# Kernel optimization log

Measured on AMD Instinct MI355X. Metric: run time of the kernel, lower is better.

## Reference

```python
import jax, jax.numpy as jnp
import numpy as np

NF = 64      # feature channels
DG = 8       # deformable groups
K = 9        # 3x3 kernel taps


def conv3(x, w, b):
    # 3x3 conv, stride 1, pad 1, NCHW/OIHW
    y = jax.lax.conv_general_dilated(x, w, (1, 1), ((1, 1), (1, 1)),
                                     dimension_numbers=('NCHW', 'OIHW', 'NCHW'))
    return y + b[None, :, None, None]


def lrelu(x):
    return jnp.where(x >= 0, x, 0.1 * x)


def up2(x):
    # matches F.interpolate(scale_factor=2, mode='bilinear', align_corners=False)
    b, c, h, w = x.shape
    return jax.image.resize(x, (b, c, 2 * h, 2 * w), method='bilinear')


def _sample_group(img, py, px):
    # img: [Cg,H,W]; py,px: [K,H,W] absolute float sample coords; zero pad outside
    H, W = img.shape[-2:]
    y0 = jnp.floor(py)
    x0 = jnp.floor(px)
    wy = py - y0
    wx = px - x0
    y0i = y0.astype(jnp.int32)
    x0i = x0.astype(jnp.int32)

    def gather(yi, xi):
        valid = (yi >= 0) & (yi < H) & (xi >= 0) & (xi < W)
        yc = jnp.clip(yi, 0, H - 1)
        xc = jnp.clip(xi, 0, W - 1)
        return img[:, yc, xc] * valid[None].astype(img.dtype)  # [Cg,K,H,W]

    v00 = gather(y0i, x0i)
    v01 = gather(y0i, x0i + 1)
    v10 = gather(y0i + 1, x0i)
    v11 = gather(y0i + 1, x0i + 1)
    return (1 - wy) * ((1 - wx) * v00 + wx * v01) + wy * ((1 - wx) * v10 + wx * v11)


def dcn_sep(x, off_fea, om_w, om_b, w, b):
    # DCN_sep: conv_offset_mask(off_fea) -> (o1,o2,mask); modulated deformable 3x3 conv on x
    B, C, H, W = x.shape
    om = conv3(off_fea, om_w, om_b)                       # [B, 3*DG*K, H, W]
    o1, o2, m = jnp.split(om, 3, axis=1)
    off_y = o1.reshape(B, DG, K, H, W)
    off_x = o2.reshape(B, DG, K, H, W)
    mask = jax.nn.sigmoid(m).reshape(B, DG, K, H, W)

    k = jnp.arange(3, dtype=x.dtype) - 1.0
    dy = jnp.repeat(k, 3)   # [K] row-major kernel offsets
    dx = jnp.tile(k, 3)
    hh = jnp.arange(H, dtype=x.dtype)
    ww = jnp.arange(W, dtype=x.dtype)
    py = off_y + dy[:, None, None] + hh[None, :, None]    # [B,DG,K,H,W]
    px = off_x + dx[:, None, None] + ww[None, None, :]

    xg = x.reshape(B, DG, C // DG, H, W)
    samp = jax.vmap(jax.vmap(_sample_group))(xg, py, px)  # [B,DG,Cg,K,H,W]
    samp = (samp * mask[:, :, None]).reshape(B, C, K, H, W)
    wk = w.reshape(w.shape[0], C, K)                      # [O,C,9]
    return jnp.einsum('ock,bckhw->bohw', wk, samp) + b[None, :, None, None]


def setup_inputs() -> dict:
    key = jax.random.key(0)
    ks = jax.random.split(key, 16)
    d = {
        'fea1_l1': jax.random.normal(ks[0], (4, NF, 128, 128), jnp.float32),
        'fea1_l2': jax.random.normal(ks[1], (4, NF, 64, 64), jnp.float32),
        'fea1_l3': jax.random.normal(ks[2], (4, NF, 32, 32), jnp.float32),
        'fea2_l1': jax.random.normal(ks[3], (4, NF, 128, 128), jnp.float32),
        'fea2_l2': jax.random.normal(ks[4], (4, NF, 64, 64), jnp.float32),
        'fea2_l3': jax.random.normal(ks[5], (4, NF, 32, 32), jnp.float32),
        # 8 plain 3x3 convs with in=2*nf: [L3_off1, L2_off1, L2_off2, L2_fea, L1_off1, L1_off2, L1_fea, cas_off1]
        'w128': jax.random.normal(ks[6], (8, NF, 2 * NF, 3, 3), jnp.float32) * 0.05,
        'b128': jax.random.normal(ks[7], (8, NF), jnp.float32) * 0.01,
        # 4 plain 3x3 convs with in=nf: [L3_off2, L2_off3, L1_off3, cas_off2]
        'w64': jax.random.normal(ks[8], (4, NF, NF, 3, 3), jnp.float32) * 0.05,
        'b64': jax.random.normal(ks[9], (4, NF), jnp.float32) * 0.01,
        # 4 DCN_sep modules: [L3, L2, L1, cas]
        'om_w': jax.random.normal(ks[10], (4, 3 * DG * K, NF, 3, 3), jnp.float32) * 0.01,
        'om_b': jax.random.normal(ks[11], (4, 3 * DG * K), jnp.float32) * 0.01,
        'dcn_w': jax.random.normal(ks[12], (4, NF, NF, 3, 3), jnp.float32) * 0.05,
        'dcn_b': jax.random.normal(ks[13], (4, NF), jnp.float32) * 0.01,
    }
    return d


def reference(fea1_l1, fea1_l2, fea1_l3, fea2_l1, fea2_l2, fea2_l3,
              w128, b128, w64, b64, om_w, om_b, dcn_w, dcn_b):
    cat = lambda a, b_: jnp.concatenate([a, b_], axis=1)
    # L3
    L3_off = lrelu(conv3(cat(fea1_l3, fea2_l3), w128[0], b128[0]))
    L3_off = lrelu(conv3(L3_off, w64[0], b64[0]))
    L3_fea = lrelu(dcn_sep(fea1_l3, L3_off, om_w[0], om_b[0], dcn_w[0], dcn_b[0]))
    # L2
    L2_off = lrelu(conv3(cat(fea1_l2, fea2_l2), w128[1], b128[1]))
    L3_off_up = up2(L3_off)
    L2_off = lrelu(conv3(cat(L2_off, L3_off_up * 2), w128[2], b128[2]))
    L2_off = lrelu(conv3(L2_off, w64[1], b64[1]))
    L2_fea = dcn_sep(fea1_l2, L2_off, om_w[1], om_b[1], dcn_w[1], dcn_b[1])
    L3_fea_up = up2(L3_fea)
    L2_fea = lrelu(conv3(cat(L2_fea, L3_fea_up), w128[3], b128[3]))
    # L1
    L1_off = lrelu(conv3(cat(fea1_l1, fea2_l1), w128[4], b128[4]))
    L2_off_up = up2(L2_off)
    L1_off = lrelu(conv3(cat(L1_off, L2_off_up * 2), w128[5], b128[5]))
    L1_off = lrelu(conv3(L1_off, w64[2], b64[2]))
    L1_fea = dcn_sep(fea1_l1, L1_off, om_w[2], om_b[2], dcn_w[2], dcn_b[2])
    L2_fea_up = up2(L2_fea)
    L1_fea = conv3(cat(L1_fea, L2_fea_up), w128[6], b128[6])
    # Cascading
    off = lrelu(conv3(cat(L1_fea, fea2_l1), w128[7], b128[7]))
    off = lrelu(conv3(off, w64[3], b64[3]))
    return lrelu(dcn_sep(L1_fea, off, om_w[3], om_b[3], dcn_w[3], dcn_b[3]))
```

## Files before the change

kernel.cpp:

```cpp
#include <hip/hip_runtime.h>
#include <cstdint>
#include <cstddef>


typedef __bf16 bf16x8 __attribute__((ext_vector_type(8)));
typedef float  f32x4  __attribute__((ext_vector_type(4)));

template<int OCPAD, int C>
__global__ void wsplit_k(const float* __restrict__ src, __bf16* __restrict__ dst,
                         int OC, long total)
{
    const int per = 9 * OCPAD * C;
    long i = (long)blockIdx.x * 256 + threadIdx.x;
    if (i >= total) return;
    int n  = (int)(i / per);
    int r  = (int)(i - (long)n * per);
    int t  = r / (OCPAD * C);
    int r2 = r - t * (OCPAD * C);
    int o  = r2 / C;
    int c  = r2 - o * C;
    float v = (o < OC) ? src[(((long)n * OC + o) * C + c) * 9 + t] : 0.f;
    __bf16 h = (__bf16)v;
    __bf16 l = (__bf16)(v - (float)h);
    __bf16* d = dst + (long)n * 2 * per;
    d[r]       = h;
    d[per + r] = l;
}

__global__ void transpose_dcnw(const float* __restrict__ w, float* __restrict__ wt, long total)
{
    long i = (long)blockIdx.x * 256 + threadIdx.x;
    if (i >= total) return;
    int n = (int)(i / 36864);
    int r = (int)(i % 36864);
    int o = r / 576;
    int c = (r % 576) / 9;
    int k = r % 9;
    wt[(long)n * 36864 + ((size_t)k * 64 + c) * 64 + o] = w[i];
}

template<int C1, int C2, int NMT, int OCPAD, bool RELU>
__global__ __launch_bounds__(256)
void conv_mfma_k(const float* __restrict__ in1, const float* __restrict__ in2,
                 float scale2, const __bf16* __restrict__ wt, const float* __restrict__ bg,
                 float* __restrict__ out, int H, int W, int OCtot)
{
    constexpr int C = C1 + C2;
    constexpr int PER = 9 * OCPAD * C;
    constexpr int NCHUNK = OCPAD / (NMT * 16);
    const int bz = blockIdx.z;
    const int b = bz / NCHUNK, chunk = bz - b * NCHUNK;
    const int ocblk = chunk * NMT * 16;
    const int tid = threadIdx.x;
    const int wid = __builtin_amdgcn_readfirstlane(tid >> 6);
    const int lane = tid & 63;
    const int pix = lane & 15;
    const int oct = lane >> 4;
    const int h0 = blockIdx.y * 8, w0 = blockIdx.x * 8;
    const size_t HW = (size_t)H * W;

    __shared__ __bf16 XH[100 * 40];
    __shared__ __bf16 XL[100 * 40];

    f32x4 accm[NMT], accc[NMT];
#pragma unroll
    for (int mt = 0; mt < NMT; ++mt) { accm[mt] = f32x4{0,0,0,0}; accc[mt] = f32x4{0,0,0,0}; }

    const int py = 2 * wid + (pix >> 3), px = pix & 7;
    const int pixbase = (py * 10 + px) * 40 + oct * 8;
    const int alane = (lane & 15) * C + oct * 8;

    for (int c0 = 0; c0 < C; c0 += 32) {
        __syncthreads();
        for (int task = tid; task < 400; task += 256) {
            int p  = task >> 2, o8 = (task & 3) * 8;
            int y  = p / 10, x = p - y * 10;
            int gy = h0 + y - 1, gx = w0 + x - 1;
            bool valid = (gy >= 0) & (gy < H) & (gx >= 0) & (gx < W);
            int cc = c0 + o8;
            const float* src; float sc;
            if (C2 == 0 || cc < C1) { src = in1 + ((size_t)b * C1 + cc) * HW; sc = 1.f; }
            else                    { src = in2 + ((size_t)b * C2 + (cc - C1)) * HW; sc = scale2; }
            const size_t gofs = (size_t)gy * W + gx;
            bf16x8 hv, lv;
#pragma unroll
            for (int j = 0; j < 8; ++j) {
                float v = valid ? src[(size_t)j * HW + gofs] * sc : 0.f;
                __bf16 h = (__bf16)v;
                hv[j] = h;
                lv[j] = (__bf16)(v - (float)h);
            }
            *(bf16x8*)(&XH[p * 40 + o8]) = hv;
            *(bf16x8*)(&XL[p * 40 + o8]) = lv;
        }
        __syncthreads();

#pragma unroll
        for (int dy = 0; dy < 3; ++dy) {
#pragma unroll
            for (int dx = 0; dx < 3; ++dx) {
                const int t = dy * 3 + dx;
                const int loff = pixbase + (dy * 10 + dx) * 40;
                bf16x8 bh = *(const bf16x8*)(&XH[loff]);
                bf16x8 bl = *(const bf16x8*)(&XL[loff]);
                const __bf16* wbase = wt + (size_t)(t * OCPAD + ocblk) * C + c0 + alane;
#pragma unroll
                for (int mt = 0; mt < NMT; ++mt) {
                    bf16x8 ah = *(const bf16x8*)(wbase + mt * 16 * C);
                    bf16x8 al = *(const bf16x8*)(wbase + mt * 16 * C + PER);
                    accm[mt] = __builtin_amdgcn_mfma_f32_16x16x32_bf16(ah, bh, accm[mt], 0, 0, 0);
                    accc[mt] = __builtin_amdgcn_mfma_f32_16x16x32_bf16(ah, bl, accc[mt], 0, 0, 0);
                    accc[mt] = __builtin_amdgcn_mfma_f32_16x16x32_bf16(al, bh, accc[mt], 0, 0, 0);
                }
            }
        }
    }

    const int orow4 = oct * 4;
    float* obase = out + (size_t)b * OCtot * HW + (size_t)(h0 + py) * W + (w0 + px);
#pragma unroll
    for (int mt = 0; mt < NMT; ++mt) {
#pragma unroll
        for (int j = 0; j < 4; ++j) {
            int oc = ocblk + mt * 16 + orow4 + j;
            if (oc < OCtot) {
                float r = accm[mt][j] + accc[mt][j] + bg[oc];
                if (RELU) r = (r >= 0.f) ? r : 0.1f * r;
                obase[(size_t)oc * HW] = r;
            }
        }
    }
}

template<bool RELU>
__global__ __launch_bounds__(256)
void dcn_k(const float* __restrict__ x, const float* __restrict__ om,
           const float* __restrict__ Wt, const float* __restrict__ bg,
           float* __restrict__ out, int H, int W)
{
    const int b = blockIdx.z;
    const int tid = threadIdx.x;
    const int wid = __builtin_amdgcn_readfirstlane(tid >> 6);
    const int p = tid & 63;
    const int h = blockIdx.y * 8 + (p >> 3), w = blockIdx.x * 8 + (p & 7);
    const size_t HW = (size_t)H * W;

    float acc[64];
#pragma unroll
    for (int o = 0; o < 64; ++o) acc[o] = 0.f;

    const float* omb = om + (size_t)b * 216 * HW + (size_t)h * W + w;
    const float* xb  = x + (size_t)b * 64 * HW;

    for (int gg = 0; gg < 2; ++gg) {
        const int g = wid * 2 + gg;
        for (int k = 0; k < 9; ++k) {
            const int ch = g * 9 + k;
            float oy = omb[(size_t)ch * HW];
            float ox = omb[(size_t)(72 + ch) * HW];
            float mr = omb[(size_t)(144 + ch) * HW];
            float m  = 1.f / (1.f + expf(-mr));

            float pyf = oy + (float)(k / 3 - 1) + (float)h;
            float pxf = ox + (float)(k % 3 - 1) + (float)w;
            float fy = floorf(pyf), fx = floorf(pxf);
            float wy = pyf - fy, wx = pxf - fx;
            int y0 = (int)fy, x0 = (int)fx;
            int y1 = y0 + 1, x1 = x0 + 1;
            bool vy0 = (y0 >= 0) & (y0 < H), vy1 = (y1 >= 0) & (y1 < H);
            bool vx0 = (x0 >= 0) & (x0 < W), vx1 = (x1 >= 0) & (x1 < W);
            int y0c = y0 < 0 ? 0 : (y0 >= H ? H - 1 : y0);
            int y1c = y1 < 0 ? 0 : (y1 >= H ? H - 1 : y1);
            int x0c = x0 < 0 ? 0 : (x0 >= W ? W - 1 : x0);
            int x1c = x1 < 0 ? 0 : (x1 >= W ? W - 1 : x1);
            float w00 = (1.f - wy) * (1.f - wx) * m * ((vy0 & vx0) ? 1.f : 0.f);
            float w01 = (1.f - wy) * wx         * m * ((vy0 & vx1) ? 1.f : 0.f);
            float w10 = wy         * (1.f - wx) * m * ((vy1 & vx0) ? 1.f : 0.f);
            float w11 = wy         * wx         * m * ((vy1 & vx1) ? 1.f : 0.f);
            size_t i00 = (size_t)y0c * W + x0c, i01 = (size_t)y0c * W + x1c;
            size_t i10 = (size_t)y1c * W + x0c, i11 = (size_t)y1c * W + x1c;

            float s[8];
#pragma unroll
            for (int cg = 0; cg < 8; ++cg) {
                const float* xc = xb + (size_t)(g * 8 + cg) * HW;
                s[cg] = w00 * xc[i00] + w01 * xc[i01] + w10 * xc[i10] + w11 * xc[i11];
            }
#pragma unroll
            for (int cg = 0; cg < 8; ++cg) {
                const float* wko = Wt + ((size_t)k * 64 + g * 8 + cg) * 64;
                float sv = s[cg];
#pragma unroll
                for (int o = 0; o < 64; ++o)
                    acc[o] = fmaf(wko[o], sv, acc[o]);
            }
        }
    }

    __shared__ float red[3][64][65];
    if (wid > 0) {
#pragma unroll
        for (int o = 0; o < 64; ++o) red[wid - 1][p][o] = acc[o];
    }
    __syncthreads();
    if (wid == 0) {
#pragma unroll
        for (int o = 0; o < 64; ++o)
            acc[o] += red[0][p][o] + red[1][p][o] + red[2][p][o];
        float* op = out + ((size_t)b * 64) * HW + (size_t)h * W + w;
#pragma unroll
        for (int o = 0; o < 64; ++o) {
            float r = acc[o] + bg[o];
            if (RELU) r = (r >= 0.f) ? r : 0.1f * r;
            op[(size_t)o * HW] = r;
        }
    }
}

__global__ void up2_k(const float* __restrict__ in, float* __restrict__ out,
                      int H, int W, long total)
{
    long idx = (long)blockIdx.x * 256 + threadIdx.x;
    if (idx >= total) return;
    const int W2 = 2 * W, H2 = 2 * H;
    int w2 = (int)(idx % W2);
    long t = idx / W2;
    int h2 = (int)(t % H2);
    long bc = t / H2;
    const float* src = in + bc * (size_t)H * W;
    int jx = w2 >> 1, jy = h2 >> 1;
    int x0, y0; float wx0, wy0;
    if (w2 & 1) { x0 = jx;     wx0 = 0.75f; } else { x0 = jx - 1; wx0 = 0.25f; }
    if (h2 & 1) { y0 = jy;     wy0 = 0.75f; } else { y0 = jy - 1; wy0 = 0.25f; }
    int x1 = x0 + 1 > W - 1 ? W - 1 : x0 + 1;
    int y1 = y0 + 1 > H - 1 ? H - 1 : y0 + 1;
    if (x0 < 0) x0 = 0;
    if (y0 < 0) y0 = 0;
    float v00 = src[(size_t)y0 * W + x0], v01 = src[(size_t)y0 * W + x1];
    float v10 = src[(size_t)y1 * W + x0], v11 = src[(size_t)y1 * W + x1];
    float wx1 = 1.f - wx0, wy1 = 1.f - wy0;
    out[idx] = wy0 * (wx0 * v00 + wx1 * v01) + wy1 * (wx0 * v10 + wx1 * v11);
}

extern "C" void kernel_launch(void* const* d_in, const int* in_sizes, int n_in,
                              void* d_out, int out_size, void* d_ws, size_t ws_size,
                              hipStream_t stream)
{
    const float* fea1_l1 = (const float*)d_in[0];
    const float* fea1_l2 = (const float*)d_in[1];
    const float* fea1_l3 = (const float*)d_in[2];
    const float* fea2_l1 = (const float*)d_in[3];
    const float* fea2_l2 = (const float*)d_in[4];
    const float* fea2_l3 = (const float*)d_in[5];
    const float* w128  = (const float*)d_in[6];
    const float* b128  = (const float*)d_in[7];
    const float* w64   = (const float*)d_in[8];
    const float* b64   = (const float*)d_in[9];
    const float* om_w  = (const float*)d_in[10];
    const float* om_b  = (const float*)d_in[11];
    const float* dcn_w = (const float*)d_in[12];
    const float* dcn_b = (const float*)d_in[13];
    float* outp = (float*)d_out;

    float* ws = (float*)d_ws;
    const size_t S1  = (size_t)4 * 64 * 128 * 128;
    const size_t S2  = (size_t)4 * 64 * 64 * 64;
    const size_t S3  = (size_t)4 * 64 * 32 * 32;
    const size_t ASZ = (size_t)4 * 216 * 128 * 128;
    float* A  = ws;
    float* Bb = ws + S1;
    float* Cb = ws + 2 * S1;
    float* Db = ws + 3 * S1;
    float* sA = ws + 4 * S1;
    float* sG = sA + ASZ - 2 * S2;
    float* sH = sA + ASZ - S2;
    float* dT = sA + ASZ;

    __bf16* U = (__bf16*)d_out;
    __bf16* w128T = U;
    __bf16* w64T  = U + 1179648;
    __bf16* omT   = U + 1474560;

    float* e3a = A;   float* e3b = A + S3;   float* e3c = A + 2 * S3;
    float* f2a = Bb;  float* f2b = Bb + S2;  float* f2c = Bb + 2 * S2;

    const dim3 blk(256);

    {
        long t1 = 8l * 73728;
        wsplit_k<64,128><<<(int)((t1 + 255) / 256), 256, 0, stream>>>(w128, w128T, 64, t1);
        long t2 = 4l * 36864;
        wsplit_k<64,64><<<(int)((t2 + 255) / 256), 256, 0, stream>>>(w64, w64T, 64, t2);
        long t3 = 4l * 129024;
        wsplit_k<224,64><<<(int)((t3 + 255) / 256), 256, 0, stream>>>(om_w, omT, 216, t3);
        transpose_dcnw<<<(int)((4l * 36864 + 255) / 256), 256, 0, stream>>>(dcn_w, dT, 4l * 36864);
    }

    conv_mfma_k<64,64,4,64,true ><<<dim3(4,4,4), blk, 0, stream>>>(fea1_l3, fea2_l3, 1.f, w128T + 0l*147456, b128 + 0*64, e3a, 32, 32, 64);
    conv_mfma_k<64, 0,4,64,true ><<<dim3(4,4,4), blk, 0, stream>>>(e3a, nullptr, 1.f, w64T + 0l*73728, b64 + 0*64, e3b, 32, 32, 64);
    conv_mfma_k<64, 0,7,224,false><<<dim3(4,4,8), blk, 0, stream>>>(e3b, nullptr, 1.f, omT + 0l*258048, om_b + 0*216, sA, 32, 32, 216);
    dcn_k<true ><<<dim3(4,4,4), blk, 0, stream>>>(fea1_l3, sA, dT + 0*36864, dcn_b + 0*64, e3c, 32, 32);

    conv_mfma_k<64,64,4,64,true ><<<dim3(8,8,4), blk, 0, stream>>>(fea1_l2, fea2_l2, 1.f, w128T + 1l*147456, b128 + 1*64, f2a, 64, 64, 64);
    up2_k<<<(int)((S2 + 255) / 256), 256, 0, stream>>>(e3b, f2b, 32, 32, (long)S2);
    conv_mfma_k<64,64,4,64,true ><<<dim3(8,8,4), blk, 0, stream>>>(f2a, f2b, 2.f, w128T + 2l*147456, b128 + 2*64, f2c, 64, 64, 64);
    conv_mfma_k<64, 0,4,64,true ><<<dim3(8,8,4), blk, 0, stream>>>(f2c, nullptr, 1.f, w64T + 1l*73728, b64 + 1*64, sG, 64, 64, 64);
    conv_mfma_k<64, 0,7,224,false><<<dim3(8,8,8), blk, 0, stream>>>(sG, nullptr, 1.f, omT + 1l*258048, om_b + 1*216, sA, 64, 64, 216);
    dcn_k<false><<<dim3(8,8,4), blk, 0, stream>>>(fea1_l2, sA, dT + 1*36864, dcn_b + 1*64, f2a, 64, 64);
    up2_k<<<(int)((S2 + 255) / 256), 256, 0, stream>>>(e3c, f2b, 32, 32, (long)S2);
    conv_mfma_k<64,64,4,64,true ><<<dim3(8,8,4), blk, 0, stream>>>(f2a, f2b, 1.f, w128T + 3l*147456, b128 + 3*64, sH, 64, 64, 64);

    conv_mfma_k<64,64,4,64,true ><<<dim3(16,16,4), blk, 0, stream>>>(fea1_l1, fea2_l1, 1.f, w128T + 4l*147456, b128 + 4*64, A, 128, 128, 64);
    up2_k<<<(int)((S1 + 255) / 256), 256, 0, stream>>>(sG, Bb, 64, 64, (long)S1);
    conv_mfma_k<64,64,4,64,true ><<<dim3(16,16,4), blk, 0, stream>>>(A, Bb, 2.f, w128T + 5l*147456, b128 + 5*64, Cb, 128, 128, 64);
    conv_mfma_k<64, 0,4,64,true ><<<dim3(16,16,4), blk, 0, stream>>>(Cb, nullptr, 1.f, w64T + 2l*73728, b64 + 2*64, A, 128, 128, 64);
    up2_k<<<(int)((S1 + 255) / 256), 256, 0, stream>>>(sH, Bb, 64, 64, (long)S1);
    conv_mfma_k<64, 0,7,224,false><<<dim3(16,16,8), blk, 0, stream>>>(A, nullptr, 1.f, omT + 2l*258048, om_b + 2*216, sA, 128, 128, 216);
    dcn_k<false><<<dim3(16,16,4), blk, 0, stream>>>(fea1_l1, sA, dT + 2*36864, dcn_b + 2*64, Cb, 128, 128);
    conv_mfma_k<64,64,4,64,false><<<dim3(16,16,4), blk, 0, stream>>>(Cb, Bb, 1.f, w128T + 6l*147456, b128 + 6*64, Db, 128, 128, 64);

    conv_mfma_k<64,64,4,64,true ><<<dim3(16,16,4), blk, 0, stream>>>(Db, fea2_l1, 1.f, w128T + 7l*147456, b128 + 7*64, A, 128, 128, 64);
    conv_mfma_k<64, 0,4,64,true ><<<dim3(16,16,4), blk, 0, stream>>>(A, nullptr, 1.f, w64T + 3l*73728, b64 + 3*64, Bb, 128, 128, 64);
    conv_mfma_k<64, 0,7,224,false><<<dim3(16,16,8), blk, 0, stream>>>(Bb, nullptr, 1.f, omT + 3l*258048, om_b + 3*216, sA, 128, 128, 216);
    dcn_k<true ><<<dim3(16,16,4), blk, 0, stream>>>(Db, sA, dT + 3*36864, dcn_b + 3*64, outp, 128, 128);
}
```

Measured before the change: 2.438 ms.

## Switch intermediates to NHWC split-bf16 and drop LDS staging in conv

All intermediate activations are converted once to NHWC hi/lo bf16 pairs. The conv kernel now loads MFMA operands straight from global memory with contiguous 8-channel vectors instead of staging and splitting fp32 NCHW tiles in LDS. Upsample, DCN sampling and the offset conv output also use NHWC, so the DCN gathers 8 channels per corner in one vector load. The aim is to remove the repeated fp32-to-bf16 split and the strided NCHW gathers, at the cost of extra conversion kernels, a reworked workspace layout, and losing the 3x3 halo reuse that LDS used to provide.

```diff
diff --git a/kernel.cpp b/kernel.cpp
--- a/kernel.cpp
+++ b/kernel.cpp
@@ -4,6 +4,7 @@
 
 
 typedef __bf16 bf16x8 __attribute__((ext_vector_type(8)));
+typedef __bf16 bf16x4 __attribute__((ext_vector_type(4)));
 typedef float  f32x4  __attribute__((ext_vector_type(4)));
 
 template<int OCPAD, int C>
@@ -39,126 +40,200 @@
     wt[(long)n * 36864 + ((size_t)k * 64 + c) * 64 + o] = w[i];
 }
 
-template<int C1, int C2, int NMT, int OCPAD, bool RELU>
+__global__ void tobf_k(const float* __restrict__ in, __bf16* __restrict__ out,
+                       long npl, int HW, long total)
+{
+    long idx = (long)blockIdx.x * 256 + threadIdx.x;
+    if (idx >= total) return;
+    int  p  = (int)(idx % HW);
+    long r  = idx / HW;
+    int  o8 = ((int)(r & 7)) * 8;
+    int  b  = (int)(r >> 3);
+    const float* src = in + ((long)b * 64 + o8) * HW + p;
+    long obase = ((long)b * HW + p) * 64 + o8;
+    bf16x8 hv, lv;
+#pragma unroll
+    for (int j = 0; j < 8; ++j) {
+        float v = src[(long)j * HW];
+        __bf16 h = (__bf16)v;
+        hv[j] = h;
+        lv[j] = (__bf16)(v - (float)h);
+    }
+    *(bf16x8*)(out + obase) = hv;
+    *(bf16x8*)(out + npl + obase) = lv;
+}
+
+__global__ void up2_nhwc_k(const __bf16* __restrict__ in, long inpl,
+                           __bf16* __restrict__ out, long outpl,
+                           int H, int W, float scale, long total)
+{
+    long idx = (long)blockIdx.x * 256 + threadIdx.x;
+    if (idx >= total) return;
+    int o8 = ((int)(idx & 7)) * 8;
+    long t = idx >> 3;
+    const int W2 = 2 * W, H2 = 2 * H;
+    int ox = (int)(t % W2); t /= W2;
+    int oy = (int)(t % H2);
+    int b  = (int)(t / H2);
+    int jx = ox >> 1, jy = oy >> 1;
+    int x0, y0; float wx0, wy0;
+    if (ox & 1) { x0 = jx;     wx0 = 0.75f; } else { x0 = jx - 1; wx0 = 0.25f; }
+    if (oy & 1) { y0 = jy;     wy0 = 0.75f; } else { y0 = jy - 1; wy0 = 0.25f; }
+    int x1 = x0 + 1 > W - 1 ? W - 1 : x0 + 1;
+    int y1 = y0 + 1 > H - 1 ? H - 1 : y0 + 1;
+    if (x0 < 0) x0 = 0;
+    if (y0 < 0) y0 = 0;
+    float v00[8], v01[8], v10[8], v11[8];
+    auto ld = [&](int yy, int xx, float* v) {
+        long bo = ((long)(b * H + yy) * W + xx) * 64 + o8;
+        bf16x8 hh = *(const bf16x8*)(in + bo);
+        bf16x8 ll = *(const bf16x8*)(in + inpl + bo);
+#pragma unroll
+        for (int j = 0; j < 8; ++j) v[j] = (float)hh[j] + (float)ll[j];
+    };
+    ld(y0, x0, v00); ld(y0, x1, v01); ld(y1, x0, v10); ld(y1, x1, v11);
+    float wx1 = 1.f - wx0, wy1 = 1.f - wy0;
+    long obo = ((long)(b * H2 + oy) * W2 + ox) * 64 + o8;
+    bf16x8 ho, lo_;
+#pragma unroll
+    for (int j = 0; j < 8; ++j) {
+        float r = (wy0 * (wx0 * v00[j] + wx1 * v01[j]) +
+                   wy1 * (wx0 * v10[j] + wx1 * v11[j])) * scale;
+        __bf16 h = (__bf16)r;
+        ho[j]  = h;
+        lo_[j] = (__bf16)(r - (float)h);
+    }
+    *(bf16x8*)(out + obo) = ho;
+    *(bf16x8*)(out + outpl + obo) = lo_;
+}
+
+template<int C, int NMT, int OCPAD, int OCTOT, bool RELU, bool OUTF32>
 __global__ __launch_bounds__(256)
-void conv_mfma_k(const float* __restrict__ in1, const float* __restrict__ in2,
-                 float scale2, const __bf16* __restrict__ wt, const float* __restrict__ bg,
-                 float* __restrict__ out, int H, int W, int OCtot)
-{
-    constexpr int C = C1 + C2;
+void conv_nhwc_k(const __bf16* __restrict__ in1, const __bf16* __restrict__ in2,
+                 long nplane, const __bf16* __restrict__ wt, const float* __restrict__ bg,
+                 void* __restrict__ outv, long onplane, int H, int W)
+{
     constexpr int PER = 9 * OCPAD * C;
-    constexpr int NCHUNK = OCPAD / (NMT * 16);
-    const int bz = blockIdx.z;
-    const int b = bz / NCHUNK, chunk = bz - b * NCHUNK;
+    const int chunk = blockIdx.z;
     const int ocblk = chunk * NMT * 16;
     const int tid = threadIdx.x;
     const int wid = __builtin_amdgcn_readfirstlane(tid >> 6);
     const int lane = tid & 63;
-    const int pix = lane & 15;
-    const int oct = lane >> 4;
-    const int h0 = blockIdx.y * 8, w0 = blockIdx.x * 8;
-    const size_t HW = (size_t)H * W;
-
-    __shared__ __bf16 XH[100 * 40];
-    __shared__ __bf16 XL[100 * 40];
-
-    f32x4 accm[NMT], accc[NMT];
-#pragma unroll
-    for (int mt = 0; mt < NMT; ++mt) { accm[mt] = f32x4{0,0,0,0}; accc[mt] = f32x4{0,0,0,0}; }
-
-    const int py = 2 * wid + (pix >> 3), px = pix & 7;
-    const int pixbase = (py * 10 + px) * 40 + oct * 8;
-    const int alane = (lane & 15) * C + oct * 8;
+    const int pix = lane & 15, oct = lane >> 4;
+    const int by = blockIdx.y * 4 + wid;
+    const int b = by / H, y = by - b * H;
+    const int x0 = blockIdx.x * 16;
+    const int x = x0 + pix;
+
+    int xoff[3]; bool vxm[3];
+#pragma unroll
+    for (int dx = 0; dx < 3; ++dx) {
+        int gx = x + dx - 1;
+        bool v = (gx >= 0) & (gx < W);
+        vxm[dx] = v;
+        int gc = v ? gx : (gx < 0 ? 0 : W - 1);
+        xoff[dx] = gc * 64;
+    }
+
+    f32x4 am[NMT], ac[NMT];
+#pragma unroll
+    for (int mt = 0; mt < NMT; ++mt) { am[mt] = f32x4{0,0,0,0}; ac[mt] = f32x4{0,0,0,0}; }
+
+    const bf16x8 zv = bf16x8{};
+    const int coctB = oct * 8;
 
     for (int c0 = 0; c0 < C; c0 += 32) {
-        __syncthreads();
-        for (int task = tid; task < 400; task += 256) {
-            int p  = task >> 2, o8 = (task & 3) * 8;
-            int y  = p / 10, x = p - y * 10;
-            int gy = h0 + y - 1, gx = w0 + x - 1;
-            bool valid = (gy >= 0) & (gy < H) & (gx >= 0) & (gx < W);
-            int cc = c0 + o8;
-            const float* src; float sc;
-            if (C2 == 0 || cc < C1) { src = in1 + ((size_t)b * C1 + cc) * HW; sc = 1.f; }
-            else                    { src = in2 + ((size_t)b * C2 + (cc - C1)) * HW; sc = scale2; }
-            const size_t gofs = (size_t)gy * W + gx;
-            bf16x8 hv, lv;
-#pragma unroll
-            for (int j = 0; j < 8; ++j) {
-                float v = valid ? src[(size_t)j * HW + gofs] * sc : 0.f;
-                __bf16 h = (__bf16)v;
-                hv[j] = h;
-                lv[j] = (__bf16)(v - (float)h);
-            }
-            *(bf16x8*)(&XH[p * 40 + o8]) = hv;
-            *(bf16x8*)(&XL[p * 40 + o8]) = lv;
+        const __bf16* src = (C == 64 || c0 < 64) ? in1 : in2;
+        const int csub = (C == 64) ? c0 : (c0 & 63);
+        const __bf16* srcl = src + nplane;
+        const int cofs = csub + coctB;
+#pragma unroll
+        for (int r = 0; r < 3; ++r) {
+            int gy = y + r - 1;
+            if (gy < 0 || gy >= H) continue;
+            long rb = ((long)(b * H + gy) * W) * 64 + cofs;
+            bf16x8 bh[3], bl[3];
+#pragma unroll
+            for (int dx = 0; dx < 3; ++dx) {
+                bf16x8 h = *(const bf16x8*)(src  + rb + xoff[dx]);
+                bf16x8 l = *(const bf16x8*)(srcl + rb + xoff[dx]);
+                bh[dx] = vxm[dx] ? h : zv;
+                bl[dx] = vxm[dx] ? l : zv;
+            }
+#pragma unroll
+            for (int dx = 0; dx < 3; ++dx) {
+                const int t = r * 3 + dx;
+                const __bf16* wb = wt + ((long)t * OCPAD + ocblk + pix) * C + c0 + coctB;
+#pragma unroll
+                for (int mt = 0; mt < NMT; ++mt) {
+                    bf16x8 ah = *(const bf16x8*)(wb + (long)mt * 16 * C);
+                    bf16x8 al = *(const bf16x8*)(wb + (long)mt * 16 * C + PER);
+                    am[mt] = __builtin_amdgcn_mfma_f32_16x16x32_bf16(ah, bh[dx], am[mt], 0, 0, 0);
+                    ac[mt] = __builtin_amdgcn_mfma_f32_16x16x32_bf16(ah, bl[dx], ac[mt], 0, 0, 0);
+                    ac[mt] = __builtin_amdgcn_mfma_f32_16x16x32_bf16(al, bh[dx], ac[mt], 0, 0, 0);
+                }
+            }
         }
-        __syncthreads();
-
-#pragma unroll
-        for (int dy = 0; dy < 3; ++dy) {
-#pragma unroll
-            for (int dx = 0; dx < 3; ++dx) {
-                const int t = dy * 3 + dx;
-                const int loff = pixbase + (dy * 10 + dx) * 40;
-                bf16x8 bh = *(const bf16x8*)(&XH[loff]);
-                bf16x8 bl = *(const bf16x8*)(&XL[loff]);
-                const __bf16* wbase = wt + (size_t)(t * OCPAD + ocblk) * C + c0 + alane;
-#pragma unroll
-                for (int mt = 0; mt < NMT; ++mt) {
-                    bf16x8 ah = *(const bf16x8*)(wbase + mt * 16 * C);
-                    bf16x8 al = *(const bf16x8*)(wbase + mt * 16 * C + PER);
-                    accm[mt] = __builtin_amdgcn_mfma_f32_16x16x32_bf16(ah, bh, accm[mt], 0, 0, 0);
-                    accc[mt] = __builtin_amdgcn_mfma_f32_16x16x32_bf16(ah, bl, accc[mt], 0, 0, 0);
-                    accc[mt] = __builtin_amdgcn_mfma_f32_16x16x32_bf16(al, bh, accc[mt], 0, 0, 0);
-                }
+    }
+
+    if (OUTF32) {
+        float* outf = (float*)outv;
+        long opix = ((long)(b * H + y) * W + x) * (long)OCTOT;
+#pragma unroll
+        for (int mt = 0; mt < NMT; ++mt) {
+#pragma unroll
+            for (int j = 0; j < 4; ++j) {
+                int oc = ocblk + mt * 16 + oct * 4 + j;
+                if (oc < OCTOT) outf[opix + oc] = am[mt][j] + ac[mt][j] + bg[oc];
             }
         }
-    }
-
-    const int orow4 = oct * 4;
-    float* obase = out + (size_t)b * OCtot * HW + (size_t)(h0 + py) * W + (w0 + px);
-#pragma unroll
-    for (int mt = 0; mt < NMT; ++mt) {
-#pragma unroll
-        for (int j = 0; j < 4; ++j) {
-            int oc = ocblk + mt * 16 + orow4 + j;
-            if (oc < OCtot) {
-                float r = accm[mt][j] + accc[mt][j] + bg[oc];
-                if (RELU) r = (r >= 0.f) ? r : 0.1f * r;
-                obase[(size_t)oc * HW] = r;
-            }
+    } else {
+        __bf16* outp = (__bf16*)outv;
+        long opix = ((long)(b * H + y) * W + x) * 64;
+#pragma unroll
+        for (int mt = 0; mt < NMT; ++mt) {
+            int oc0 = ocblk + mt * 16 + oct * 4;
+            bf16x4 hv, lv;
+#pragma unroll
+            for (int j = 0; j < 4; ++j) {
+                float rv = am[mt][j] + ac[mt][j] + bg[oc0 + j];
+                if (RELU) rv = (rv >= 0.f) ? rv : 0.1f * rv;
+                __bf16 hh = (__bf16)rv;
+                hv[j] = hh;
+                lv[j] = (__bf16)(rv - (float)hh);
+            }
+            *(bf16x4*)(outp + opix + oc0) = hv;
+            *(bf16x4*)(outp + onplane + opix + oc0) = lv;
         }
     }
 }
 
-template<bool RELU>
+template<bool RELU, bool OUTF32>
 __global__ __launch_bounds__(256)
-void dcn_k(const float* __restrict__ x, const float* __restrict__ om,
-           const float* __restrict__ Wt, const float* __restrict__ bg,
-           float* __restrict__ out, int H, int W)
+void dcn_nhwc_k(const __bf16* __restrict__ x, long xnpl,
+                const float* __restrict__ om,
+                const float* __restrict__ Wt, const float* __restrict__ bg,
+                void* __restrict__ outv, long onpl, int H, int W)
 {
     const int b = blockIdx.z;
     const int tid = threadIdx.x;
     const int wid = __builtin_amdgcn_readfirstlane(tid >> 6);
     const int p = tid & 63;
     const int h = blockIdx.y * 8 + (p >> 3), w = blockIdx.x * 8 + (p & 7);
-    const size_t HW = (size_t)H * W;
 
     float acc[64];
 #pragma unroll
     for (int o = 0; o < 64; ++o) acc[o] = 0.f;
 
-    const float* omb = om + (size_t)b * 216 * HW + (size_t)h * W + w;
-    const float* xb  = x + (size_t)b * 64 * HW;
+    const float* omp = om + ((long)(b * H + h) * W + w) * 216;
 
     for (int gg = 0; gg < 2; ++gg) {
         const int g = wid * 2 + gg;
         for (int k = 0; k < 9; ++k) {
             const int ch = g * 9 + k;
-            float oy = omb[(size_t)ch * HW];
-            float ox = omb[(size_t)(72 + ch) * HW];
-            float mr = omb[(size_t)(144 + ch) * HW];
+            float oy = omp[ch];
+            float ox = omp[72 + ch];
+            float mr = omp[144 + ch];
             float m  = 1.f / (1.f + expf(-mr));
 
             float pyf = oy + (float)(k / 3 - 1) + (float)h;
@@ -177,18 +252,28 @@
             float w01 = (1.f - wy) * wx         * m * ((vy0 & vx1) ? 1.f : 0.f);
             float w10 = wy         * (1.f - wx) * m * ((vy1 & vx0) ? 1.f : 0.f);
             float w11 = wy         * wx         * m * ((vy1 & vx1) ? 1.f : 0.f);
-            size_t i00 = (size_t)y0c * W + x0c, i01 = (size_t)y0c * W + x1c;
-            size_t i10 = (size_t)y1c * W + x0c, i11 = (size_t)y1c * W + x1c;
+
+            long i00 = ((long)(b * H + y0c) * W + x0c) * 64 + g * 8;
+            long i01 = ((long)(b * H + y0c) * W + x1c) * 64 + g * 8;
+            long i10 = ((long)(b * H + y1c) * W + x0c) * 64 + g * 8;
+            long i11 = ((long)(b * H + y1c) * W + x1c) * 64 + g * 8;
+
+            bf16x8 h00 = *(const bf16x8*)(x + i00), l00 = *(const bf16x8*)(x + xnpl + i00);
+            bf16x8 h01 = *(const bf16x8*)(x + i01), l01 = *(const bf16x8*)(x + xnpl + i01);
+            bf16x8 h10 = *(const bf16x8*)(x + i10), l10 = *(const bf16x8*)(x + xnpl + i10);
+            bf16x8 h11 = *(const bf16x8*)(x + i11), l11 = *(const bf16x8*)(x + xnpl + i11);
 
             float s[8];
 #pragma unroll
+            for (int j = 0; j < 8; ++j) {
+                s[j] = w00 * ((float)h00[j] + (float)l00[j])
+                     + w01 * ((float)h01[j] + (float)l01[j])
+                     + w10 * ((float)h10[j] + (float)l10[j])
+                     + w11 * ((float)h11[j] + (float)l11[j]);
+            }
+#pragma unroll
             for (int cg = 0; cg < 8; ++cg) {
-                const float* xc = xb + (size_t)(g * 8 + cg) * HW;
-                s[cg] = w00 * xc[i00] + w01 * xc[i01] + w10 * xc[i10] + w11 * xc[i11];
-            }
-#pragma unroll
-            for (int cg = 0; cg < 8; ++cg) {
-                const float* wko = Wt + ((size_t)k * 64 + g * 8 + cg) * 64;
+                const float* wko = Wt + ((long)k * 64 + g * 8 + cg) * 64;
                 float sv = s[cg];
 #pragma unroll
                 for (int o = 0; o < 64; ++o)
@@ -207,39 +292,34 @@
 #pragma unroll
         for (int o = 0; o < 64; ++o)
             acc[o] += red[0][p][o] + red[1][p][o] + red[2][p][o];
-        float* op = out + ((size_t)b * 64) * HW + (size_t)h * W + w;
-#pragma unroll
-        for (int o = 0; o < 64; ++o) {
-            float r = acc[o] + bg[o];
-            if (RELU) r = (r >= 0.f) ? r : 0.1f * r;
-            op[(size_t)o * HW] = r;
+        if (OUTF32) {
+            const long HW = (long)H * W;
+            float* op = (float*)outv + ((long)b * 64) * HW + (long)h * W + w;
+#pragma unroll
+            for (int o = 0; o < 64; ++o) {
+                float r = acc[o] + bg[o];
+                if (RELU) r = (r >= 0.f) ? r : 0.1f * r;
+                op[(long)o * HW] = r;
+            }
+        } else {
+            __bf16* op = (__bf16*)outv;
+            long obo = ((long)(b * H + h) * W + w) * 64;
+#pragma unroll
+            for (int o0 = 0; o0 < 64; o0 += 8) {
+                bf16x8 hv, lv;
+#pragma unroll
+                for (int j = 0; j < 8; ++j) {
+                    float r = acc[o0 + j] + bg[o0 + j];
+                    if (RELU) r = (r >= 0.f) ? r : 0.1f * r;
+                    __bf16 hh = (__bf16)r;
+                    hv[j] = hh;
+                    lv[j] = (__bf16)(r - (float)hh);
+                }
+                *(bf16x8*)(op + obo + o0) = hv;
+                *(bf16x8*)(op + onpl + obo + o0) = lv;
+            }
         }
     }
-}
-
-__global__ void up2_k(const float* __restrict__ in, float* __restrict__ out,
-                      int H, int W, long total)
-{
-    long idx = (long)blockIdx.x * 256 + threadIdx.x;
-    if (idx >= total) return;
-    const int W2 = 2 * W, H2 = 2 * H;
-    int w2 = (int)(idx % W2);
-    long t = idx / W2;
-    int h2 = (int)(t % H2);
-    long bc = t / H2;
-    const float* src = in + bc * (size_t)H * W;
-    int jx = w2 >> 1, jy = h2 >> 1;
-    int x0, y0; float wx0, wy0;
-    if (w2 & 1) { x0 = jx;     wx0 = 0.75f; } else { x0 = jx - 1; wx0 = 0.25f; }
-    if (h2 & 1) { y0 = jy;     wy0 = 0.75f; } else { y0 = jy - 1; wy0 = 0.25f; }
-    int x1 = x0 + 1 > W - 1 ? W - 1 : x0 + 1;
-    int y1 = y0 + 1 > H - 1 ? H - 1 : y0 + 1;
-    if (x0 < 0) x0 = 0;
-    if (y0 < 0) y0 = 0;
-    float v00 = src[(size_t)y0 * W + x0], v01 = src[(size_t)y0 * W + x1];
-    float v10 = src[(size_t)y1 * W + x0], v11 = src[(size_t)y1 * W + x1];
-    float wx1 = 1.f - wx0, wy1 = 1.f - wy0;
-    out[idx] = wy0 * (wx0 * v00 + wx1 * v01) + wy1 * (wx0 * v10 + wx1 * v11);
 }
 
 extern "C" void kernel_launch(void* const* d_in, const int* in_sizes, int n_in,
@@ -260,67 +340,94 @@
     const float* om_b  = (const float*)d_in[11];
     const float* dcn_w = (const float*)d_in[12];
     const float* dcn_b = (const float*)d_in[13];
-    float* outp = (float*)d_out;
-
+
+    const long NPL1 = 4194304, NPL2 = 1048576, NPL3 = 262144;
     float* ws = (float*)d_ws;
-    const size_t S1  = (size_t)4 * 64 * 128 * 128;
-    const size_t S2  = (size_t)4 * 64 * 64 * 64;
-    const size_t S3  = (size_t)4 * 64 * 32 * 32;
-    const size_t ASZ = (size_t)4 * 216 * 128 * 128;
-    float* A  = ws;
-    float* Bb = ws + S1;
-    float* Cb = ws + 2 * S1;
-    float* Db = ws + 3 * S1;
-    float* sA = ws + 4 * S1;
-    float* sG = sA + ASZ - 2 * S2;
-    float* sH = sA + ASZ - S2;
-    float* dT = sA + ASZ;
-
-    __bf16* U = (__bf16*)d_out;
-    __bf16* w128T = U;
-    __bf16* w64T  = U + 1179648;
-    __bf16* omT   = U + 1474560;
-
-    float* e3a = A;   float* e3b = A + S3;   float* e3c = A + 2 * S3;
-    float* f2a = Bb;  float* f2b = Bb + S2;  float* f2c = Bb + 2 * S2;
-
-    const dim3 blk(256);
-
-    {
-        long t1 = 8l * 73728;
-        wsplit_k<64,128><<<(int)((t1 + 255) / 256), 256, 0, stream>>>(w128, w128T, 64, t1);
-        long t2 = 4l * 36864;
-        wsplit_k<64,64><<<(int)((t2 + 255) / 256), 256, 0, stream>>>(w64, w64T, 64, t2);
-        long t3 = 4l * 129024;
-        wsplit_k<224,64><<<(int)((t3 + 255) / 256), 256, 0, stream>>>(om_w, omT, 216, t3);
-        transpose_dcnw<<<(int)((4l * 36864 + 255) / 256), 256, 0, stream>>>(dcn_w, dT, 4l * 36864);
-    }
-
-    conv_mfma_k<64,64,4,64,true ><<<dim3(4,4,4), blk, 0, stream>>>(fea1_l3, fea2_l3, 1.f, w128T + 0l*147456, b128 + 0*64, e3a, 32, 32, 64);
-    conv_mfma_k<64, 0,4,64,true ><<<dim3(4,4,4), blk, 0, stream>>>(e3a, nullptr, 1.f, w64T + 0l*73728, b64 + 0*64, e3b, 32, 32, 64);
-    conv_mfma_k<64, 0,7,224,false><<<dim3(4,4,8), blk, 0, stream>>>(e3b, nullptr, 1.f, omT + 0l*258048, om_b + 0*216, sA, 32, 32, 216);
-    dcn_k<true ><<<dim3(4,4,4), blk, 0, stream>>>(fea1_l3, sA, dT + 0*36864, dcn_b + 0*64, e3c, 32, 32);
-
-    conv_mfma_k<64,64,4,64,true ><<<dim3(8,8,4), blk, 0, stream>>>(fea1_l2, fea2_l2, 1.f, w128T + 1l*147456, b128 + 1*64, f2a, 64, 64, 64);
-    up2_k<<<(int)((S2 + 255) / 256), 256, 0, stream>>>(e3b, f2b, 32, 32, (long)S2);
-    conv_mfma_k<64,64,4,64,true ><<<dim3(8,8,4), blk, 0, stream>>>(f2a, f2b, 2.f, w128T + 2l*147456, b128 + 2*64, f2c, 64, 64, 64);
-    conv_mfma_k<64, 0,4,64,true ><<<dim3(8,8,4), blk, 0, stream>>>(f2c, nullptr, 1.f, w64T + 1l*73728, b64 + 1*64, sG, 64, 64, 64);
-    conv_mfma_k<64, 0,7,224,false><<<dim3(8,8,8), blk, 0, stream>>>(sG, nullptr, 1.f, omT + 1l*258048, om_b + 1*216, sA, 64, 64, 216);
-    dcn_k<false><<<dim3(8,8,4), blk, 0, stream>>>(fea1_l2, sA, dT + 1*36864, dcn_b + 1*64, f2a, 64, 64);
-    up2_k<<<(int)((S2 + 255) / 256), 256, 0, stream>>>(e3c, f2b, 32, 32, (long)S2);
-    conv_mfma_k<64,64,4,64,true ><<<dim3(8,8,4), blk, 0, stream>>>(f2a, f2b, 1.f, w128T + 3l*147456, b128 + 3*64, sH, 64, 64, 64);
-
-    conv_mfma_k<64,64,4,64,true ><<<dim3(16,16,4), blk, 0, stream>>>(fea1_l1, fea2_l1, 1.f, w128T + 4l*147456, b128 + 4*64, A, 128, 128, 64);
-    up2_k<<<(int)((S1 + 255) / 256), 256, 0, stream>>>(sG, Bb, 64, 64, (long)S1);
-    conv_mfma_k<64,64,4,64,true ><<<dim3(16,16,4), blk, 0, stream>>>(A, Bb, 2.f, w128T + 5l*147456, b128 + 5*64, Cb, 128, 128, 64);
-    conv_mfma_k<64, 0,4,64,true ><<<dim3(16,16,4), blk, 0, stream>>>(Cb, nullptr, 1.f, w64T + 2l*73728, b64 + 2*64, A, 128, 128, 64);
-    up2_k<<<(int)((S1 + 255) / 256), 256, 0, stream>>>(sH, Bb, 64, 64, (long)S1);
-    conv_mfma_k<64, 0,7,224,false><<<dim3(16,16,8), blk, 0, stream>>>(A, nullptr, 1.f, omT + 2l*258048, om_b + 2*216, sA, 128, 128, 216);
-    dcn_k<false><<<dim3(16,16,4), blk, 0, stream>>>(fea1_l1, sA, dT + 2*36864, dcn_b + 2*64, Cb, 128, 128);
-    conv_mfma_k<64,64,4,64,false><<<dim3(16,16,4), blk, 0, stream>>>(Cb, Bb, 1.f, w128T + 6l*147456, b128 + 6*64, Db, 128, 128, 64);
-
-    conv_mfma_k<64,64,4,64,true ><<<dim3(16,16,4), blk, 0, stream>>>(Db, fea2_l1, 1.f, w128T + 7l*147456, b128 + 7*64, A, 128, 128, 64);
-    conv_mfma_k<64, 0,4,64,true ><<<dim3(16,16,4), blk, 0, stream>>>(A, nullptr, 1.f, w64T + 3l*73728, b64 + 3*64, Bb, 128, 128, 64);
-    conv_mfma_k<64, 0,7,224,false><<<dim3(16,16,8), blk, 0, stream>>>(Bb, nullptr, 1.f, omT + 3l*258048, om_b + 3*216, sA, 128, 128, 216);
-    dcn_k<true ><<<dim3(16,16,4), blk, 0, stream>>>(Db, sA, dT + 3*36864, dcn_b + 3*64, outp, 128, 128);
-}
+    auto bfp = [&](long woff) -> __bf16* { return (__bf16*)(ws + woff); };
+
+    const long Z_OM   = 0;
+    const long Z_A1   = 0;
+    const long Z_A2   = 4194304;
+    const long Z_F1L3 = 1048576, Z_F2L3 = 1310720;
+    const long Z_F1L2 = 3538944, Z_F2L2 = 4587520;
+    const long Z_A2L2 = 4587520;
+    const long Z_SG   = 7340032;
+    const long Z_SH   = 8388608;
+    const long Z_SF   = 9437184;
+    const long Z_SE   = 9699328;
+    const long Z_S1   = 14155776;
+    const long Z_S2   = 18350080;
+    const long Z_F1L1 = 22544384, Z_F2L1 = 26738688;
+    const long Z_WB   = 30932992;
+    const long Z_DT   = 32186368;
+
+    __bf16* wsp   = (__bf16*)(ws + Z_WB);
+    __bf16* w128T = wsp;
+    __bf16* w64T  = wsp + 1179648;
+    __bf16* omT   = wsp + 1474560;
+    float*  dT    = ws + Z_DT;
+    float*  omB   = ws + Z_OM;
+    float*  outp  = (float*)d_out;
+    __bf16* dscr  = (__bf16*)d_out;
+
+    auto blocks = [](long n) { return (int)((n + 255) / 256); };
+
+    { long t = 8l * 73728;  wsplit_k<64,128><<<blocks(t), 256, 0, stream>>>(w128, w128T, 64, t); }
+    { long t = 4l * 36864;  wsplit_k<64,64 ><<<blocks(t), 256, 0, stream>>>(w64,  w64T,  64, t); }
+    { long t = 4l * 129024; wsplit_k<224,64><<<blocks(t), 256, 0, stream>>>(om_w, omT,  216, t); }
+    transpose_dcnw<<<blocks(4l * 36864), 256, 0, stream>>>(dcn_w, dT, 4l * 36864);
+
+    tobf_k<<<blocks(4l*8*16384), 256, 0, stream>>>(fea1_l1, bfp(Z_F1L1), NPL1, 16384, 4l*8*16384);
+    tobf_k<<<blocks(4l*8*16384), 256, 0, stream>>>(fea2_l1, bfp(Z_F2L1), NPL1, 16384, 4l*8*16384);
+    tobf_k<<<blocks(4l*8*4096),  256, 0, stream>>>(fea1_l2, bfp(Z_F1L2), NPL2, 4096,  4l*8*4096);
+    tobf_k<<<blocks(4l*8*4096),  256, 0, stream>>>(fea2_l2, bfp(Z_F2L2), NPL2, 4096,  4l*8*4096);
+    tobf_k<<<blocks(4l*8*1024),  256, 0, stream>>>(fea1_l3, bfp(Z_F1L3), NPL3, 1024,  4l*8*1024);
+    tobf_k<<<blocks(4l*8*1024),  256, 0, stream>>>(fea2_l3, bfp(Z_F2L3), NPL3, 1024,  4l*8*1024);
+
+    conv_nhwc_k<128,4,64,64,true,false><<<dim3(2,32,1), 256, 0, stream>>>(
+        bfp(Z_F1L3), bfp(Z_F2L3), NPL3, w128T + 0l*147456, b128 + 0*64, bfp(Z_S1), NPL3, 32, 32);
+    conv_nhwc_k<64,4,64,64,true,false><<<dim3(2,32,1), 256, 0, stream>>>(
+        bfp(Z_S1), nullptr, NPL3, w64T + 0l*73728, b64 + 0*64, bfp(Z_SE), NPL3, 32, 32);
+    conv_nhwc_k<64,7,224,216,false,true><<<dim3(2,32,2), 256, 0, stream>>>(
+        bfp(Z_SE), nullptr, NPL3, omT + 0l*258048, om_b + 0*216, omB, 0, 32, 32);
+    dcn_nhwc_k<true,false><<<dim3(4,4,4), 256, 0, stream>>>(
+        bfp(Z_F1L3), NPL3, omB, dT + 0*36864, dcn_b + 0*64, bfp(Z_SF), NPL3, 32, 32);
+
+    conv_nhwc_k<128,4,64,64,true,false><<<dim3(4,64,1), 256, 0, stream>>>(
+        bfp(Z_F1L2), bfp(Z_F2L2), NPL2, w128T + 1l*147456, b128 + 1*64, bfp(Z_S1), NPL2, 64, 64);
+    up2_nhwc_k<<<blocks(4l*8*4096), 256, 0, stream>>>(bfp(Z_SE), NPL3, bfp(Z_S2), NPL2, 32, 32, 2.f, 4l*8*4096);
+    conv_nhwc_k<128,4,64,64,true,false><<<dim3(4,64,1), 256, 0, stream>>>(
+        bfp(Z_S1), bfp(Z_S2), NPL2, w128T + 2l*147456, b128 + 2*64, bfp(Z_A2L2), NPL2, 64, 64);
+    conv_nhwc_k<64,4,64,64,true,false><<<dim3(4,64,1), 256, 0, stream>>>(
+        bfp(Z_A2L2), nullptr, NPL2, w64T + 1l*73728, b64 + 1*64, bfp(Z_SG), NPL2, 64, 64);
+    conv_nhwc_k<64,7,224,216,false,true><<<dim3(4,64,2), 256, 0, stream>>>(
+        bfp(Z_SG), nullptr, NPL2, omT + 1l*258048, om_b + 1*216, omB, 0, 64, 64);
+    dcn_nhwc_k<false,false><<<dim3(8,8,4), 256, 0, stream>>>(
+        bfp(Z_F1L2), NPL2, omB, dT + 1*36864, dcn_b + 1*64, bfp(Z_S1), NPL2, 64, 64);
+    up2_nhwc_k<<<blocks(4l*8*4096), 256, 0, stream>>>(bfp(Z_SF), NPL3, bfp(Z_S2), NPL2, 32, 32, 1.f, 4l*8*4096);
+    conv_nhwc_k<128,4,64,64,true,false><<<dim3(4,64,1), 256, 0, stream>>>(
+        bfp(Z_S1), bfp(Z_S2), NPL2, w128T + 3l*147456, b128 + 3*64, bfp(Z_SH), NPL2, 64, 64);
+
+    conv_nhwc_k<128,4,64,64,true,false><<<dim3(8,128,1), 256, 0, stream>>>(
+        bfp(Z_F1L1), bfp(Z_F2L1), NPL1, w128T + 4l*147456, b128 + 4*64, bfp(Z_A1), NPL1, 128, 128);
+    up2_nhwc_k<<<blocks(4l*8*16384), 256, 0, stream>>>(bfp(Z_SG), NPL2, bfp(Z_S1), NPL1, 64, 64, 2.f, 4l*8*16384);
+    conv_nhwc_k<128,4,64,64,true,false><<<dim3(8,128,1), 256, 0, stream>>>(
+        bfp(Z_A1), bfp(Z_S1), NPL1, w128T + 5l*147456, b128 + 5*64, bfp(Z_A2), NPL1, 128, 128);
+    conv_nhwc_k<64,4,64,64,true,false><<<dim3(8,128,1), 256, 0, stream>>>(
+        bfp(Z_A2), nullptr, NPL1, w64T + 2l*73728, b64 + 2*64, bfp(Z_S1), NPL1, 128, 128);
+    up2_nhwc_k<<<blocks(4l*8*16384), 256, 0, stream>>>(bfp(Z_SH), NPL2, dscr, NPL1, 64, 64, 1.f, 4l*8*16384);
+    conv_nhwc_k<64,7,224,216,false,true><<<dim3(8,128,2), 256, 0, stream>>>(
+        bfp(Z_S1), nullptr, NPL1, omT + 2l*258048, om_b + 2*216, omB, 0, 128, 128);
+    dcn_nhwc_k<false,false><<<dim3(16,16,4), 256, 0, stream>>>(
+        bfp(Z_F1L1), NPL1, omB, dT + 2*36864, dcn_b + 2*64, bfp(Z_S2), NPL1, 128, 128);
+    conv_nhwc_k<128,4,64,64,false,false><<<dim3(8,128,1), 256, 0, stream>>>(
+        bfp(Z_S2), dscr, NPL1, w128T + 6l*147456, b128 + 6*64, bfp(Z_S1), NPL1, 128, 128);
+    conv_nhwc_k<128,4,64,64,true,false><<<dim3(8,128,1), 256, 0, stream>>>(
+        bfp(Z_S1), bfp(Z_F2L1), NPL1, w128T + 7l*147456, b128 + 7*64, bfp(Z_S2), NPL1, 128, 128);
+    conv_nhwc_k<64,4,64,64,true,false><<<dim3(8,128,1), 256, 0, stream>>>(
+        bfp(Z_S2), nullptr, NPL1, w64T + 3l*73728, b64 + 3*64, dscr, NPL1, 128, 128);
+    conv_nhwc_k<64,7,224,216,false,true><<<dim3(8,128,2), 256, 0, stream>>>(
+        dscr, nullptr, NPL1, omT + 3l*258048, om_b + 3*216, omB, 0, 128, 128);
+    dcn_nhwc_k<true,true><<<dim3(16,16,4), 256, 0, stream>>>(
+        bfp(Z_S1), NPL1, omB, dT + 3*36864, dcn_b + 3*64, outp, 0, 128, 128);
+}
```

Measured after the change: 2.546 ms. 4.4% more time.
